# Kernel optimization log

Hardware: AMD Instinct MI355X
Metric: run time of the kernel (lower is better)

Reference implementation:

```python
import jax, jax.numpy as jnp
import numpy as np

N = 400_000      # total nodes in batched graph
E = 6_400_000    # total edges (avg degree 16)
G = 6_400        # total small graphs
B = 64           # samples; num[i] graphs per sample, sum(num)=G
F = 31           # feature dim (hard-coded in TAG)
K = 2            # TAGConv hops
L = 5            # number of TAGConv layers
MAXG = 120       # max graphs per sample (120*31 pad)


def setup_inputs() -> dict:
    key = jax.random.key(0)
    ks = jax.random.split(key, 8)
    x = jax.random.normal(ks[0], (N, F), dtype=jnp.float32)
    src = jax.random.randint(ks[1], (E,), 0, N, dtype=jnp.int32)
    dst = jax.random.randint(ks[2], (E,), 0, N, dtype=jnp.int32)
    # contiguous (sorted) graph assignment, every graph non-empty (~62 nodes each)
    graph_ids = jnp.asarray((np.arange(N, dtype=np.int64) * G) // N, dtype=jnp.int32)
    num = jnp.full((B,), G // B, dtype=jnp.int32)  # 100 graphs per sample
    Ws = jax.random.normal(ks[3], (L, (K + 1) * F, F), dtype=jnp.float32) * 0.1
    bs = jax.random.normal(ks[4], (L, F), dtype=jnp.float32) * 0.01
    w_gate = jax.random.normal(ks[5], (F,), dtype=jnp.float32) * 0.1
    b_gate = jax.random.normal(ks[6], (1,), dtype=jnp.float32) * 0.01
    return {"x": x, "Ws": Ws, "bs": bs, "w_gate": w_gate, "b_gate": b_gate,
            "src": src, "dst": dst, "graph_ids": graph_ids, "num": num}


def reference(x, Ws, bs, w_gate, b_gate, src, dst, graph_ids, num):
    # symmetric normalization: norm = in_deg^{-1/2}, deg clamped to >=1 (DGL TAGConv)
    deg = jax.ops.segment_sum(jnp.ones((E,), x.dtype), dst, num_segments=N)
    norm = jnp.clip(deg, 1.0, None) ** -0.5  # [N]

    def tagconv(h, W, b):
        fstack = [h]
        cur = h
        for _ in range(K):
            cur = norm[:, None] * cur
            cur = jax.ops.segment_sum(cur[src], dst, num_segments=N)  # SPMM hop
            cur = norm[:, None] * cur
            fstack.append(cur)
        return jnp.concatenate(fstack, axis=-1) @ W + b  # [N, F]

    h = x
    for l in range(L):
        h = jax.nn.relu(tagconv(h, Ws[l], bs[l]))

    # GlobalAttentionPooling: segment softmax over gate scores, weighted sum
    gate = h @ w_gate + b_gate[0]                                   # [N]
    gmax = jax.ops.segment_max(gate, graph_ids, num_segments=G)     # [G]
    e = jnp.exp(gate - gmax[graph_ids])
    den = jax.ops.segment_sum(e, graph_ids, num_segments=G)
    alpha = e / den[graph_ids]
    rep = jax.ops.segment_sum(alpha[:, None] * h, graph_ids, num_segments=G)  # [G, F]

    # split by num, flatten, pad to 120*31, stack
    csum = jnp.cumsum(num)
    offsets = jnp.concatenate([jnp.zeros((1,), jnp.int32), csum.astype(jnp.int32)])
    g = jnp.arange(G, dtype=jnp.int32)
    sample_id = jnp.searchsorted(csum, g, side="right").astype(jnp.int32)  # [G]
    pos = g - offsets[sample_id]
    out = jnp.zeros((B, MAXG, F), rep.dtype).at[sample_id, pos].set(rep)
    return out.reshape(B, MAXG * F)
```

## Files before the change

### kernel.cpp

```cpp
#include <hip/hip_runtime.h>
#include <hip/hip_bf16.h>

#define FDIM 31
#define FPAD 32
#define RSTRIDE 16

#define CBITS 11
#define CW    (1 << CBITS)
#define MAXBUK 256
#define TILE 4096

typedef int      iv4 __attribute__((ext_vector_type(4)));
typedef unsigned uv4 __attribute__((ext_vector_type(4)));

__device__ __forceinline__ float bf_lo(unsigned u) { return __uint_as_float(u << 16); }
__device__ __forceinline__ float bf_hi(unsigned u) { return __uint_as_float(u & 0xFFFF0000u); }
__device__ __forceinline__ unsigned pack2(float lo, float hi) {
    unsigned a = __float_as_uint(lo), b = __float_as_uint(hi);
    unsigned ra = (a + 0x7FFFu + ((a >> 16) & 1u)) >> 16;
    unsigned rb = (b + 0x7FFFu + ((b >> 16) & 1u)) >> 16;
    return ra | (rb << 16);
}

__device__ __forceinline__ int lb_gid(const int* __restrict__ gid, int Ntot, int g) {
    int lo = 0, hi = Ntot;
    while (lo < hi) { int mid = (lo + hi) >> 1; if (gid[mid] < g) lo = mid + 1; else hi = mid; }
    return lo;
}

__global__ __launch_bounds__(256) void multisplit_kernel(
    const int* __restrict__ src, const int* __restrict__ dst,
    int* __restrict__ gcnt, int* __restrict__ bucketed,
    int cap, int E, int nbuk)
{
    __shared__ int ordered[TILE];
    __shared__ int hist[MAXBUK];
    __shared__ int lofs[MAXBUK + 1];
    __shared__ int base_[MAXBUK];
    __shared__ int cur[MAXBUK];
    const int tid = threadIdx.x;
    const int e0 = blockIdx.x * TILE;
    const int n = min(TILE, E - e0);
    if (tid < MAXBUK) hist[tid] = 0;
    __syncthreads();
    for (int i = tid; i < n; i += 256)
        atomicAdd(&hist[dst[e0 + i] >> CBITS], 1);
    __syncthreads();
    if (tid == 0) {
        int a = 0;
        for (int b = 0; b < nbuk; ++b) { lofs[b] = a; a += hist[b]; }
        lofs[nbuk] = a;
    }
    __syncthreads();
    if (tid < nbuk) {
        int h = hist[tid];
        base_[tid] = h ? atomicAdd(&gcnt[tid], h) : 0;
        cur[tid] = lofs[tid];
    }
    __syncthreads();
    for (int i = tid; i < n; i += 256) {
        int s = src[e0 + i], d = dst[e0 + i];
        int b = d >> CBITS;
        int r = atomicAdd(&cur[b], 1);
        ordered[r] = (s << CBITS) | (d & (CW - 1));
    }
    __syncthreads();
    for (int i = tid; i < n; i += 256) {
        int lo = 0, hi = nbuk;
        while (hi - lo > 1) {
            int mid = (lo + hi) >> 1;
            if (lofs[mid] <= i) lo = mid; else hi = mid;
        }
        int b = lo;
        int pos = base_[b] + (i - lofs[b]);
        if (pos < cap) bucketed[(size_t)b * cap + pos] = ordered[i];
    }
}

__global__ void small_scans_kernel(const int* __restrict__ num, int* __restrict__ soff, int Bn,
                                   const int* __restrict__ gcnt, int* __restrict__ bbase,
                                   int nbuk, int cap) {
    if (threadIdx.x == 0 && blockIdx.x == 0) {
        int acc = 0; soff[0] = 0;
        for (int i = 0; i < Bn; ++i) { acc += num[i]; soff[i + 1] = acc; }
        int a = 0;
        for (int b = 0; b < nbuk; ++b) {
            bbase[b] = a;
            a += ((min(gcnt[b], cap) + 7) & ~7) + 7 * CW;
        }
    }
}

__global__ __launch_bounds__(1024) void bucket_build_kernel(
    const int* __restrict__ bucketed, const int* __restrict__ gcnt,
    const int* __restrict__ bbase,
    int* __restrict__ rowbeg, int* __restrict__ rowend,
    float* __restrict__ normv, float* __restrict__ invn,
    int* __restrict__ col,
    int cap, int N, int nbuk)
{
    __shared__ int hist[CW];
    __shared__ int lcur[CW];
    const int b = blockIdx.x, tid = threadIdx.x;
    hist[tid] = 0; hist[tid + 1024] = 0;
    __syncthreads();
    const int cnt = min(gcnt[b], cap);
    const int* reg = bucketed + (size_t)b * cap;
    for (int i = tid; i < cnt; i += 1024)
        atomicAdd(&hist[reg[i] & (CW - 1)], 1);
    __syncthreads();
    int c0 = hist[tid], c1 = hist[tid + 1024];
    int p0 = (c0 + 7) & ~7, p1 = (c1 + 7) & ~7;
    __syncthreads();
    hist[tid] = p0; hist[tid + 1024] = p1;
    __syncthreads();
    for (int off = 1; off < CW; off <<= 1) {
        int a0 = (tid >= off) ? hist[tid - off] : 0;
        int a1 = (tid + 1024 >= off) ? hist[tid + 1024 - off] : 0;
        __syncthreads();
        hist[tid] += a0; hist[tid + 1024] += a1;
        __syncthreads();
    }
    const int base = bbase[b];
    const int base_node = b << CBITS;
    int r0 = -1, r1 = -1;
    int node = base_node + tid;
    if (node < N) {
        r0 = base + hist[tid] - p0;
        rowbeg[node] = r0; rowend[node] = r0 + p0; lcur[tid] = r0;
        int cr = c0 > 0 ? c0 : 1;
        normv[node] = rsqrtf((float)cr);
        invn[node]  = sqrtf((float)cr);
    }
    node = base_node + tid + 1024;
    if (node < N) {
        r1 = base + hist[tid + 1024] - p1;
        rowbeg[node] = r1; rowend[node] = r1 + p1; lcur[tid + 1024] = r1;
        int cr = c1 > 0 ? c1 : 1;
        normv[node] = rsqrtf((float)cr);
        invn[node]  = sqrtf((float)cr);
    }
    __syncthreads();
    for (int i = tid; i < cnt; i += 1024) {
        int e = reg[i];
        int p = atomicAdd(&lcur[e & (CW - 1)], 1);
        col[p] = e >> CBITS;
    }
    if (r0 >= 0) for (int j = r0 + c0; j < r0 + p0; ++j) col[j] = N;
    if (r1 >= 0) for (int j = r1 + c1; j < r1 + p1; ++j) col[j] = N;
}

__global__ void cast_x_kernel(const float* __restrict__ x, const float* __restrict__ normv,
                              unsigned* __restrict__ A, int N) {
    int idx = blockIdx.x * 256 + threadIdx.x;
    if (idx >= (N + 1) * RSTRIDE) return;
    int n = idx >> 4, q = idx & 15;
    if (n >= N) { A[idx] = 0u; return; }
    float nv = normv[n];
    int f0 = 2 * q, f1 = 2 * q + 1;
    float lo = (f0 < FDIM) ? nv * x[(size_t)n * FDIM + f0] : 0.0f;
    float hi = (f1 < FDIM) ? nv * x[(size_t)n * FDIM + f1] : 0.0f;
    A[idx] = pack2(lo, hi);
}

#define GATHER8(HSRC, r0, r1, r2, r3, r4, r5, r6, r7, CA, CB)                    \
    r0 = *((const uint4*)(HSRC + (size_t)(CA).x * RSTRIDE) + sub);               \
    r1 = *((const uint4*)(HSRC + (size_t)(CA).y * RSTRIDE) + sub);               \
    r2 = *((const uint4*)(HSRC + (size_t)(CA).z * RSTRIDE) + sub);               \
    r3 = *((const uint4*)(HSRC + (size_t)(CA).w * RSTRIDE) + sub);               \
    r4 = *((const uint4*)(HSRC + (size_t)(CB).x * RSTRIDE) + sub);               \
    r5 = *((const uint4*)(HSRC + (size_t)(CB).y * RSTRIDE) + sub);               \
    r6 = *((const uint4*)(HSRC + (size_t)(CB).z * RSTRIDE) + sub);               \
    r7 = *((const uint4*)(HSRC + (size_t)(CB).w * RSTRIDE) + sub);

#define ACC_EDGE(vN)                                                   \
    acc0 += bf_lo(vN.x); acc1 += bf_hi(vN.x);                          \
    acc2 += bf_lo(vN.y); acc3 += bf_hi(vN.y);                          \
    acc4 += bf_lo(vN.z); acc5 += bf_hi(vN.z);                          \
    acc6 += bf_lo(vN.w); acc7 += bf_hi(vN.w);

#define ACC8(r0, r1, r2, r3, r4, r5, r6, r7)                           \
    ACC_EDGE(r0) ACC_EDGE(r1) ACC_EDGE(r2) ACC_EDGE(r3)                \
    ACC_EDGE(r4) ACC_EDGE(r5) ACC_EDGE(r6) ACC_EDGE(r7)

__global__ __launch_bounds__(256) void spmm_kernel(const unsigned* __restrict__ Hin,
                                                   unsigned* __restrict__ Hout,
                                                   const int* __restrict__ rowbeg,
                                                   const int* __restrict__ rowend,
                                                   const int* __restrict__ col,
                                                   const float* __restrict__ normv, int N) {
    int node = blockIdx.x * 64 + (threadIdx.x >> 2);
    int sub = threadIdx.x & 3;
    if (node > N) return;
    if (node == N) {
        uv4 z = (uv4)0;
        __builtin_nontemporal_store(z, (uv4*)(Hout + (size_t)N * RSTRIDE) + sub);
        return;
    }
    int s = rowbeg[node];
    int nit = (rowend[node] - s) >> 3;
    float acc0 = 0.f, acc1 = 0.f, acc2 = 0.f, acc3 = 0.f;
    float acc4 = 0.f, acc5 = 0.f, acc6 = 0.f, acc7 = 0.f;
    if (nit > 0) {
        const iv4* cl = (const iv4*)(col + s);
        iv4 ca = __builtin_nontemporal_load(cl);
        iv4 cb = __builtin_nontemporal_load(cl + 1);
        for (int it = 0; it < nit; ++it) {
            uint4 v0, v1, v2, v3, v4, v5, v6, v7;
            GATHER8(Hin, v0, v1, v2, v3, v4, v5, v6, v7, ca, cb)
            const iv4* nx = cl + ((it + 1 < nit) ? 2 : 0);
            iv4 na = __builtin_nontemporal_load(nx);
            iv4 nb = __builtin_nontemporal_load(nx + 1);
            cl += 2;
            ACC8(v0, v1, v2, v3, v4, v5, v6, v7)
            ca = na; cb = nb;
        }
    }
    float nv = normv[node];
    float nn2 = nv * nv;
    uv4 o;
    o.x = pack2(nn2 * acc0, nn2 * acc1);
    o.y = pack2(nn2 * acc2, nn2 * acc3);
    o.z = pack2(nn2 * acc4, nn2 * acc5);
    o.w = pack2(nn2 * acc6, nn2 * acc7);
    __builtin_nontemporal_store(o, (uv4*)(Hout + (size_t)node * RSTRIDE) + sub);
}

template<int JB, int NJ>
__device__ __forceinline__ void mlp_cols(const uint4 (&ra)[4], const uint4 (&rb)[4],
                                         const float* hp, const float* __restrict__ W,
                                         const float* __restrict__ bias,
                                         float inv, float sc, unsigned* orow,
                                         const float* __restrict__ w_gate,
                                         int do_gate, float& gp) {
    float out[8];
#pragma unroll
    for (int jj = 0; jj < 8; ++jj) out[jj] = 0.0f;
    {
        const unsigned* ru = (const unsigned*)ra;
#pragma unroll
        for (int i = 0; i < FDIM; ++i) {
            float v = (i & 1) ? bf_hi(ru[i >> 1]) : bf_lo(ru[i >> 1]);
#pragma unroll
            for (int jj = 0; jj < NJ; ++jj)
                out[jj] = fmaf(v, W[i * FDIM + JB + jj], out[jj]);
        }
    }
    {
        const unsigned* ru = (const unsigned*)rb;
#pragma unroll
        for (int i = 0; i < FDIM; ++i) {
            float v = (i & 1) ? bf_hi(ru[i >> 1]) : bf_lo(ru[i >> 1]);
#pragma unroll
            for (int jj = 0; jj < NJ; ++jj)
                out[jj] = fmaf(v, W[FDIM * FDIM + i * FDIM + JB + jj], out[jj]);
        }
    }
    {
#pragma unroll
        for (int i = 0; i < FDIM; ++i) {
            float v = hp[i];
#pragma unroll
            for (int jj = 0; jj < NJ; ++jj)
                out[jj] = fmaf(v, W[2 * FDIM * FDIM + i * FDIM + JB + jj], out[jj]);
        }
    }
#pragma unroll
    for (int jj = 0; jj < NJ; ++jj)
        out[jj] = fmaxf(fmaf(out[jj], inv, bias[JB + jj]), 0.0f);
#pragma unroll
    for (int jj = NJ; jj < 8; ++jj) out[jj] = 0.0f;
    uint4 q;
    q.x = pack2(sc * out[0], sc * out[1]);
    q.y = pack2(sc * out[2], sc * out[3]);
    q.z = pack2(sc * out[4], sc * out[5]);
    q.w = pack2(sc * out[6], sc * out[7]);
    ((uint4*)orow)[JB >> 3] = q;
    if (do_gate) {
#pragma unroll
        for (int jj = 0; jj < NJ; ++jj)
            gp = fmaf(out[jj], w_gate[JB + jj], gp);
    }
}

__global__ __launch_bounds__(256, 5) void spmm_mlp_kernel(
    const unsigned* __restrict__ Hb,
    unsigned* __restrict__ Ha,
    const int* __restrict__ rowbeg,
    const int* __restrict__ rowend,
    const int* __restrict__ col,
    const float* __restrict__ normv,
    const float* __restrict__ invn,
    const float* __restrict__ W,
    const float* __restrict__ bias,
    float* __restrict__ gatev,
    const float* __restrict__ w_gate,
    const float* __restrict__ b_gate,
    int do_gate, int N)
{
    __shared__ float hcL[64 * 33];
    __shared__ float gred[256];
    const int tid = threadIdx.x;
    {
        int node = blockIdx.x * 64 + (tid >> 2);
        int sub = tid & 3;
        if (node < N) {
            int s = rowbeg[node];
            int nit = (rowend[node] - s) >> 3;
            float acc0 = 0.f, acc1 = 0.f, acc2 = 0.f, acc3 = 0.f;
            float acc4 = 0.f, acc5 = 0.f, acc6 = 0.f, acc7 = 0.f;
            if (nit > 0) {
                const iv4* cl = (const iv4*)(col + s);
                iv4 ca = __builtin_nontemporal_load(cl);
                iv4 cb = __builtin_nontemporal_load(cl + 1);
                for (int it = 0; it < nit; ++it) {
                    uint4 v0, v1, v2, v3, v4, v5, v6, v7;
                    GATHER8(Hb, v0, v1, v2, v3, v4, v5, v6, v7, ca, cb)
                    const iv4* nx = cl + ((it + 1 < nit) ? 2 : 0);
                    iv4 na = __builtin_nontemporal_load(nx);
                    iv4 nb = __builtin_nontemporal_load(nx + 1);
                    cl += 2;
                    ACC8(v0, v1, v2, v3, v4, v5, v6, v7)
                    ca = na; cb = nb;
                }
            }
            float nv = normv[node];
            float nn2 = nv * nv;
            float* hp = &hcL[(tid >> 2) * 33 + sub * 8];
            hp[0] = nn2 * acc0; hp[1] = nn2 * acc1;
            hp[2] = nn2 * acc2; hp[3] = nn2 * acc3;
            hp[4] = nn2 * acc4; hp[5] = nn2 * acc5;
            hp[6] = nn2 * acc6; hp[7] = nn2 * acc7;
        }
    }
    __syncthreads();
    const int ln = tid & 63;
    const int wv = tid >> 6;
    const int n2 = blockIdx.x * 64 + ln;
    uint4 ra[4];
    if (n2 < N) {
        const uint4* r4p = (const uint4*)(Ha + (size_t)n2 * RSTRIDE);
#pragma unroll
        for (int q = 0; q < 4; ++q) ra[q] = r4p[q];
    }
    __syncthreads();
    float gp = 0.0f;
    if (n2 < N) {
        uint4 rb[4];
        const uint4* r4p = (const uint4*)(Hb + (size_t)n2 * RSTRIDE);
#pragma unroll
        for (int q = 0; q < 4; ++q) rb[q] = r4p[q];
        const float* hp = &hcL[ln * 33];
        float inv = invn[n2];
        float sc = do_gate ? 1.0f : normv[n2];
        unsigned* orow = Ha + (size_t)n2 * RSTRIDE;
        if      (wv == 0) mlp_cols<0,  8>(ra, rb, hp, W, bias, inv, sc, orow, w_gate, do_gate, gp);
        else if (wv == 1) mlp_cols<8,  8>(ra, rb, hp, W, bias, inv, sc, orow, w_gate, do_gate, gp);
        else if (wv == 2) mlp_cols<16, 8>(ra, rb, hp, W, bias, inv, sc, orow, w_gate, do_gate, gp);
        else              mlp_cols<24, 7>(ra, rb, hp, W, bias, inv, sc, orow, w_gate, do_gate, gp);
    }
    if (do_gate) {
        gred[tid] = gp;
        __syncthreads();
        if (tid < 64 && n2 < N)
            gatev[n2] = b_gate[0] + gred[tid] + gred[tid + 64] + gred[tid + 128] + gred[tid + 192];
    }
}


__global__ __launch_bounds__(64) void graph_reduce_kernel(const float* __restrict__ gate,
                                                          const int* __restrict__ gid,
                                                          const int* __restrict__ soff, int Bn,
                                                          int Ntot,
                                                          float* __restrict__ gmax,
                                                          float* __restrict__ gden) {
    int g = blockIdx.x;
    if (g >= soff[Bn]) return;
    int s = lb_gid(gid, Ntot, g), e = lb_gid(gid, Ntot, g + 1);
    float m = -1e30f;
    for (int n = s + threadIdx.x; n < e; n += 64) m = fmaxf(m, gate[n]);
#pragma unroll
    for (int o = 32; o > 0; o >>= 1) m = fmaxf(m, __shfl_xor(m, o));
    float d = 0.0f;
    for (int n = s + threadIdx.x; n < e; n += 64) d += expf(gate[n] - m);
#pragma unroll
    for (int o = 32; o > 0; o >>= 1) d += __shfl_xor(d, o);
    if (threadIdx.x == 0) { gmax[g] = m; gden[g] = d; }
}

__global__ __launch_bounds__(64) void rep_scatter_kernel(const unsigned short* __restrict__ H,
                                                         const float* __restrict__ gate,
                                                         const int* __restrict__ gid,
                                                         const int* __restrict__ soff,
                                                         int MAXG, int Ntot,
                                                         const float* __restrict__ gmax,
                                                         const float* __restrict__ gden,
                                                         float* __restrict__ out) {
    int s = blockIdx.x / MAXG;
    int pos = blockIdx.x % MAXG;
    int t = threadIdx.x;
    if (t >= FDIM) return;
    int gbeg = soff[s], gend = soff[s + 1];
    float* op = out + ((size_t)s * MAXG + pos) * FDIM + t;
    if (pos >= gend - gbeg) { *op = 0.0f; return; }
    int g = gbeg + pos;
    int ns = lb_gid(gid, Ntot, g), ne = lb_gid(gid, Ntot, g + 1);
    float m = gmax[g], den = gden[g];
    float acc = 0.0f;
    for (int n = ns; n < ne; ++n) {
        float hv = __uint_as_float((unsigned)H[(size_t)n * FPAD + t] << 16);
        acc += expf(gate[n] - m) * hv;
    }
    *op = acc / den;
}


extern "C" void kernel_launch(void* const* d_in, const int* in_sizes, int n_in,
                              void* d_out, int out_size, void* d_ws, size_t ws_size,
                              hipStream_t stream) {
    const float* x      = (const float*)d_in[0];
    const float* Ws     = (const float*)d_in[1];
    const float* bs     = (const float*)d_in[2];
    const float* w_gate = (const float*)d_in[3];
    const float* b_gate = (const float*)d_in[4];
    const int* src       = (const int*)d_in[5];
    const int* dst       = (const int*)d_in[6];
    const int* graph_ids = (const int*)d_in[7];
    const int* num       = (const int*)d_in[8];
    float* out  = (float*)d_out;

    const int N  = in_sizes[7];
    const int E  = in_sizes[5];
    const int Bn = in_sizes[8];
    const int F  = in_sizes[3];
    const int L  = in_sizes[2] / F;
    const int nW = in_sizes[1];
    const int WperL = nW / L;
    const int MAXG = out_size / (Bn * F);
    const int Gmax = Bn * MAXG;

    const int nbuk = (N + CW - 1) / CW;
    const int cap  = E / nbuk + E / (8 * nbuk) + 2048;

    char* p = (char*)d_ws;
    auto alloc = [&](size_t bytes) {
        void* r = (void*)p;
        p += (bytes + 255) & ~(size_t)255;
        return r;
    };
    unsigned* HA = (unsigned*)alloc((size_t)(N + 1) * RSTRIDE * 4);
    unsigned* HB = (unsigned*)alloc((size_t)(N + 1) * RSTRIDE * 4);
    int*   colw  = (int*)alloc(((size_t)E + (size_t)nbuk * (7 * CW + 16)) * 4);
    int*   bkt   = (int*)alloc((size_t)nbuk * cap * 4);
    int*   gcnt  = (int*)alloc((size_t)nbuk * 4);
    int*   bbase = (int*)alloc((size_t)nbuk * 4);
    int*   rowb  = (int*)alloc((size_t)(N + 1) * 4);
    int*   rowe  = (int*)alloc((size_t)(N + 1) * 4);
    float* normv = (float*)alloc((size_t)N * 4);
    float* invnv = (float*)alloc((size_t)N * 4);
    float* gatev = (float*)alloc((size_t)N * 4);
    float* gmax  = (float*)alloc((size_t)Gmax * 4);
    float* gden  = (float*)alloc((size_t)Gmax * 4);
    int*   soff  = (int*)alloc((size_t)(Bn + 1) * 4);

    (void)hipMemsetAsync(gcnt, 0, (size_t)nbuk * 4, stream);

    const int NT = (E + TILE - 1) / TILE;
    multisplit_kernel<<<NT, 256, 0, stream>>>(src, dst, gcnt, bkt, cap, E, nbuk);
    small_scans_kernel<<<1, 64, 0, stream>>>(num, soff, Bn, gcnt, bbase, nbuk, cap);
    bucket_build_kernel<<<nbuk, 1024, 0, stream>>>(bkt, gcnt, bbase, rowb, rowe,
                                                   normv, invnv, colw, cap, N, nbuk);

    cast_x_kernel<<<((N + 1) * RSTRIDE + 255) / 256, 256, 0, stream>>>(x, normv, HA, N);

    const int SB  = (N + 1 + 63) / 64;
    const int SB2 = (N + 63) / 64;
    for (int l = 0; l < L; ++l) {
        spmm_kernel<<<SB, 256, 0, stream>>>(HA, HB, rowb, rowe, colw, normv, N);
        spmm_mlp_kernel<<<SB2, 256, 0, stream>>>(HB, HA, rowb, rowe, colw, normv, invnv,
                                                 Ws + (size_t)l * WperL, bs + (size_t)l * F,
                                                 gatev, w_gate, b_gate,
                                                 (l == L - 1) ? 1 : 0, N);
    }

    graph_reduce_kernel<<<Gmax, 64, 0, stream>>>(gatev, graph_ids, soff, Bn, N, gmax, gden);
    rep_scatter_kernel<<<Gmax, 64, 0, stream>>>((const unsigned short*)HA, gatev, graph_ids,
                                                soff, MAXG, N, gmax, gden, out);
    (void)n_in; (void)ws_size;
}
```

Baseline: 1.556 ms.

## Overlap MLP partial products with SpMM gather and drop nontemporal stores

The fused SpMM+MLP kernel now loads the hop-0 and hop-1 rows before the gather phase and computes the first two thirds of the dense product before the barrier. Only the hop-2 part waits on shared memory after the sync. This removes one __syncthreads and lets the dense FMAs overlap gather latency, at the cost of more live registers, so the occupancy hint drops from 5 to 4 blocks. The standalone SpMM kernel also switches from nontemporal stores to normal stores, so its output can stay in cache for the next hop.

```diff
diff --git a/kernel.cpp b/kernel.cpp
--- a/kernel.cpp
+++ b/kernel.cpp
@@ -193,8 +193,8 @@
     int sub = threadIdx.x & 3;
     if (node > N) return;
     if (node == N) {
-        uv4 z = (uv4)0;
-        __builtin_nontemporal_store(z, (uv4*)(Hout + (size_t)N * RSTRIDE) + sub);
+        uint4 z; z.x = z.y = z.z = z.w = 0u;
+        *((uint4*)(Hout + (size_t)N * RSTRIDE) + sub) = z;
         return;
     }
     int s = rowbeg[node];
@@ -218,52 +218,44 @@
     }
     float nv = normv[node];
     float nn2 = nv * nv;
-    uv4 o;
+    uint4 o;
     o.x = pack2(nn2 * acc0, nn2 * acc1);
     o.y = pack2(nn2 * acc2, nn2 * acc3);
     o.z = pack2(nn2 * acc4, nn2 * acc5);
     o.w = pack2(nn2 * acc6, nn2 * acc7);
-    __builtin_nontemporal_store(o, (uv4*)(Hout + (size_t)node * RSTRIDE) + sub);
+    *((uint4*)(Hout + (size_t)node * RSTRIDE) + sub) = o;
 }
 
 template<int JB, int NJ>
-__device__ __forceinline__ void mlp_cols(const uint4 (&ra)[4], const uint4 (&rb)[4],
-                                         const float* hp, const float* __restrict__ W,
-                                         const float* __restrict__ bias,
-                                         float inv, float sc, unsigned* orow,
-                                         const float* __restrict__ w_gate,
-                                         int do_gate, float& gp) {
-    float out[8];
-#pragma unroll
-    for (int jj = 0; jj < 8; ++jj) out[jj] = 0.0f;
-    {
-        const unsigned* ru = (const unsigned*)ra;
-#pragma unroll
-        for (int i = 0; i < FDIM; ++i) {
-            float v = (i & 1) ? bf_hi(ru[i >> 1]) : bf_lo(ru[i >> 1]);
-#pragma unroll
-            for (int jj = 0; jj < NJ; ++jj)
-                out[jj] = fmaf(v, W[i * FDIM + JB + jj], out[jj]);
+__device__ __forceinline__ void mlp_pre(const uint4 (&ra)[4], const uint4 (&rb)[4],
+                                        const float* __restrict__ W, float (&out)[8]) {
+    const unsigned* ru = (const unsigned*)ra;
+    const unsigned* rv = (const unsigned*)rb;
+#pragma unroll
+    for (int i = 0; i < FDIM; ++i) {
+        float va = (i & 1) ? bf_hi(ru[i >> 1]) : bf_lo(ru[i >> 1]);
+        float vb = (i & 1) ? bf_hi(rv[i >> 1]) : bf_lo(rv[i >> 1]);
+#pragma unroll
+        for (int jj = 0; jj < NJ; ++jj) {
+            out[jj] = fmaf(va, W[i * FDIM + JB + jj], out[jj]);
+            out[jj] = fmaf(vb, W[FDIM * FDIM + i * FDIM + JB + jj], out[jj]);
         }
     }
-    {
-        const unsigned* ru = (const unsigned*)rb;
-#pragma unroll
-        for (int i = 0; i < FDIM; ++i) {
-            float v = (i & 1) ? bf_hi(ru[i >> 1]) : bf_lo(ru[i >> 1]);
-#pragma unroll
-            for (int jj = 0; jj < NJ; ++jj)
-                out[jj] = fmaf(v, W[FDIM * FDIM + i * FDIM + JB + jj], out[jj]);
-        }
-    }
-    {
-#pragma unroll
-        for (int i = 0; i < FDIM; ++i) {
-            float v = hp[i];
-#pragma unroll
-            for (int jj = 0; jj < NJ; ++jj)
-                out[jj] = fmaf(v, W[2 * FDIM * FDIM + i * FDIM + JB + jj], out[jj]);
-        }
+}
+
+template<int JB, int NJ>
+__device__ __forceinline__ void mlp_fin(float (&out)[8], const float* hp,
+                                        const float* __restrict__ W,
+                                        const float* __restrict__ bias,
+                                        float inv, float sc, unsigned* orow,
+                                        const float* __restrict__ w_gate,
+                                        int do_gate, float& gp) {
+#pragma unroll
+    for (int i = 0; i < FDIM; ++i) {
+        float v = hp[i];
+#pragma unroll
+        for (int jj = 0; jj < NJ; ++jj)
+            out[jj] = fmaf(v, W[2 * FDIM * FDIM + i * FDIM + JB + jj], out[jj]);
     }
 #pragma unroll
     for (int jj = 0; jj < NJ; ++jj)
@@ -283,7 +275,7 @@
     }
 }
 
-__global__ __launch_bounds__(256, 5) void spmm_mlp_kernel(
+__global__ __launch_bounds__(256, 4) void spmm_mlp_kernel(
     const unsigned* __restrict__ Hb,
     unsigned* __restrict__ Ha,
     const int* __restrict__ rowbeg,
@@ -301,6 +293,18 @@
     __shared__ float hcL[64 * 33];
     __shared__ float gred[256];
     const int tid = threadIdx.x;
+    const int ln = tid & 63;
+    const int wv = tid >> 6;
+    const int n2 = blockIdx.x * 64 + ln;
+    uint4 ra[4], rb[4];
+    if (n2 < N) {
+        const uint4* pa = (const uint4*)(Ha + (size_t)n2 * RSTRIDE);
+        const uint4* pb = (const uint4*)(Hb + (size_t)n2 * RSTRIDE);
+#pragma unroll
+        for (int q = 0; q < 4; ++q) ra[q] = pa[q];
+#pragma unroll
+        for (int q = 0; q < 4; ++q) rb[q] = pb[q];
+    }
     {
         int node = blockIdx.x * 64 + (tid >> 2);
         int sub = tid & 3;
@@ -333,31 +337,26 @@
             hp[6] = nn2 * acc6; hp[7] = nn2 * acc7;
         }
     }
-    __syncthreads();
-    const int ln = tid & 63;
-    const int wv = tid >> 6;
-    const int n2 = blockIdx.x * 64 + ln;
-    uint4 ra[4];
+    float out[8];
+#pragma unroll
+    for (int jj = 0; jj < 8; ++jj) out[jj] = 0.0f;
     if (n2 < N) {
-        const uint4* r4p = (const uint4*)(Ha + (size_t)n2 * RSTRIDE);
-#pragma unroll
-        for (int q = 0; q < 4; ++q) ra[q] = r4p[q];
+        if      (wv == 0) mlp_pre<0,  8>(ra, rb, W, out);
+        else if (wv == 1) mlp_pre<8,  8>(ra, rb, W, out);
+        else if (wv == 2) mlp_pre<16, 8>(ra, rb, W, out);
+        else              mlp_pre<24, 7>(ra, rb, W, out);
     }
     __syncthreads();
     float gp = 0.0f;
     if (n2 < N) {
-        uint4 rb[4];
-        const uint4* r4p = (const uint4*)(Hb + (size_t)n2 * RSTRIDE);
-#pragma unroll
-        for (int q = 0; q < 4; ++q) rb[q] = r4p[q];
         const float* hp = &hcL[ln * 33];
         float inv = invn[n2];
         float sc = do_gate ? 1.0f : normv[n2];
         unsigned* orow = Ha + (size_t)n2 * RSTRIDE;
-        if      (wv == 0) mlp_cols<0,  8>(ra, rb, hp, W, bias, inv, sc, orow, w_gate, do_gate, gp);
-        else if (wv == 1) mlp_cols<8,  8>(ra, rb, hp, W, bias, inv, sc, orow, w_gate, do_gate, gp);
-        else if (wv == 2) mlp_cols<16, 8>(ra, rb, hp, W, bias, inv, sc, orow, w_gate, do_gate, gp);
-        else              mlp_cols<24, 7>(ra, rb, hp, W, bias, inv, sc, orow, w_gate, do_gate, gp);
+        if      (wv == 0) mlp_fin<0,  8>(out, hp, W, bias, inv, sc, orow, w_gate, do_gate, gp);
+        else if (wv == 1) mlp_fin<8,  8>(out, hp, W, bias, inv, sc, orow, w_gate, do_gate, gp);
+        else if (wv == 2) mlp_fin<16, 8>(out, hp, W, bias, inv, sc, orow, w_gate, do_gate, gp);
+        else              mlp_fin<24, 7>(out, hp, W, bias, inv, sc, orow, w_gate, do_gate, gp);
     }
     if (do_gate) {
         gred[tid] = gp;
```

Measured after the change: 1.556 ms. Within noise of the previous version (+0.0%).
